# Optimization experiments

Hardware: AMD Instinct MI355X
Metric: run time of the kernel (lower is better)

## Reference

```python
import jax, jax.numpy as jnp
import numpy as np

N = 50000      # nodes
E = 800000     # edges (before self-loops)
F_IN = 256     # input features
HID = 32       # per-head hidden channels, conv1
H1 = 4         # heads conv1 (concat)
H2 = 4         # heads conv2 (mean)
NCLS = 40      # output classes
NEG_SLOPE = 0.2
SM_EPS = 1e-16  # PyG softmax denominator eps
LN_EPS = 1e-5


def setup_inputs() -> dict:
    key = jax.random.key(0)
    ks = jax.random.split(key, 12)
    s1 = 1.0 / np.sqrt(F_IN)
    s2 = 1.0 / np.sqrt(H1 * HID)
    return {
        "x": jax.random.normal(ks[0], (N, F_IN), dtype=jnp.float32),
        "edge_index": jax.random.randint(ks[1], (2, E), 0, N, dtype=jnp.int32),
        "W1": jax.random.normal(ks[2], (F_IN, H1 * HID), dtype=jnp.float32) * s1,
        "att_src1": jax.random.normal(ks[3], (H1, HID), dtype=jnp.float32) * s1,
        "att_dst1": jax.random.normal(ks[4], (H1, HID), dtype=jnp.float32) * s1,
        "b1": jnp.zeros((H1 * HID,), jnp.float32),
        "W2": jax.random.normal(ks[5], (H1 * HID, H2 * NCLS), dtype=jnp.float32) * s2,
        "att_src2": jax.random.normal(ks[6], (H2, NCLS), dtype=jnp.float32) * s2,
        "att_dst2": jax.random.normal(ks[7], (H2, NCLS), dtype=jnp.float32) * s2,
        "b2": jnp.zeros((NCLS,), jnp.float32),
        "ln0_g": jnp.ones((H1 * HID,), jnp.float32),
        "ln0_b": jnp.zeros((H1 * HID,), jnp.float32),
        "ln1_g": jnp.ones((NCLS,), jnp.float32),
        "ln1_b": jnp.zeros((NCLS,), jnp.float32),
    }


def gat_conv(x, edge_index, W, a_src, a_dst, bias, heads, ch, concat):
    """PyG GATConv: self-loops, edge attention, per-dst segment softmax, scatter-sum."""
    n = x.shape[0]
    loops = jnp.arange(n, dtype=edge_index.dtype)
    src = jnp.concatenate([edge_index[0], loops])  # message source
    dst = jnp.concatenate([edge_index[1], loops])  # aggregation target
    h = (x @ W).reshape(n, heads, ch)              # [N,H,C]
    e_src = jnp.einsum('nhc,hc->nh', h, a_src)     # [N,H]
    e_dst = jnp.einsum('nhc,hc->nh', h, a_dst)
    e = jax.nn.leaky_relu(e_src[src] + e_dst[dst], NEG_SLOPE)  # [E',H]
    m = jax.ops.segment_max(e, dst, num_segments=n)            # stable softmax max
    p = jnp.exp(e - m[dst])
    denom = jax.ops.segment_sum(p, dst, num_segments=n)
    alpha = p / (denom[dst] + SM_EPS)                          # [E',H]
    out = jax.ops.segment_sum(h[src] * alpha[:, :, None], dst, num_segments=n)  # [N,H,C]
    out = out.reshape(n, heads * ch) if concat else out.mean(axis=1)
    return out + bias


def layer_norm(x, g, b):
    mu = x.mean(axis=-1, keepdims=True)
    var = jnp.mean((x - mu) ** 2, axis=-1, keepdims=True)
    return (x - mu) * jax.lax.rsqrt(var + LN_EPS) * g + b


def reference(x, edge_index, W1, att_src1, att_dst1, b1, W2, att_src2, att_dst2, b2,
              ln0_g, ln0_b, ln1_g, ln1_b):
    # eval mode: dropout = identity
    h = gat_conv(x, edge_index, W1, att_src1, att_dst1, b1, H1, HID, True)
    h = layer_norm(jax.nn.elu(h), ln0_g, ln0_b)
    h = gat_conv(h, edge_index, W2, att_src2, att_dst2, b2, H2, NCLS, False)
    h = layer_norm(h, ln1_g, ln1_b)
    return jax.nn.log_softmax(h, axis=1)
```

## Files before the change

kernel.cpp:

```cpp
#include <hip/hip_runtime.h>
#include <hip/hip_bf16.h>
#include <hip/hip_fp16.h>

#define NNODES 50000
#define NEDGES 800000
#define FIN    256
#define HEADS  4
#define C1     32
#define D1     128
#define C2     40
#define D2     160
#define CAP    64

#define RB1 144
#define RB2 88
#define ZB  ((NNODES + 255) / 256)
#define FB  (NEDGES / 256)
#define GB1 ((NNODES + 63) / 64)

typedef unsigned short u16;
typedef short v8s __attribute__((ext_vector_type(8)));
typedef float v4f __attribute__((ext_vector_type(4)));

__device__ __forceinline__ float bf2f(unsigned u) {
    union { unsigned u; float f; } x; x.u = u << 16; return x.f;
}
__device__ __forceinline__ u16 f2bf(float f) {
    unsigned u = __float_as_uint(f);
    return (u16)((u + 0x7fff + ((u >> 16) & 1)) >> 16);
}
__device__ __forceinline__ unsigned pk_bf16(float a, float b) {
    unsigned ua = (__float_as_uint(a) + 0x8000u) >> 16;
    unsigned ub = (__float_as_uint(b) + 0x8000u) & 0xffff0000u;
    return ub | ua;
}
__device__ __forceinline__ float wave_sum(float v) {
    #pragma unroll
    for (int m = 32; m > 0; m >>= 1) v += __shfl_xor(v, m, 64);
    return v;
}
__device__ __forceinline__ void wave_sum2(float& a, float& b) {
    #pragma unroll
    for (int m = 32; m > 0; m >>= 1) {
        a += __shfl_xor(a, m, 64);
        b += __shfl_xor(b, m, 64);
    }
}
__device__ __forceinline__ float leaky(float x) { return fmaxf(x, 0.2f * x); }

__device__ __forceinline__ void repack_body(const float* __restrict__ W,
                                            const float* __restrict__ as,
                                            const float* __restrict__ ad,
                                            u16* __restrict__ Wf,
                                            int K, int N, int C, int total, int idx) {
    if (idx >= total) return;
    int KS = K >> 5, NT = N >> 4;
    int j = idx & 7, lane = (idx >> 3) & 63;
    int rest = idx >> 9;
    int ks = rest % KS, nt = rest / KS;
    int k = ks * 32 + (lane >> 4) * 8 + j;
    int n16 = lane & 15;
    float val = 0.f;
    if (nt < NT) {
        val = W[(size_t)k * N + nt * 16 + n16];
    } else if (n16 < 8) {
        int h = n16 & 3;
        const float* av = (n16 < 4) ? as : ad;
        float s = 0.f;
        for (int c = 0; c < C; c++) s += W[(size_t)k * N + h * C + c] * av[h * C + c];
        val = s;
    }
    Wf[idx] = f2bf(val);
}

template <bool AF32, int KK, int NT>
__device__ __forceinline__ void gemm_body(const void* __restrict__ Aptr,
                                          const u16* __restrict__ Wf,
                                          u16* __restrict__ Out,
                                          float* __restrict__ ssrc,
                                          float* __restrict__ sdst, int M, int bid) {
    const int KS = KK / 32;
    const int NCOL = NT * 16;
    int wid = threadIdx.x >> 6, lane = threadIdx.x & 63;
    int r0 = bid * 64 + wid * 16;
    int m = lane & 15, quad = lane >> 4;
    int row = r0 + m;
    bool rowok = row < M;

    v8s a[KS];
    if (AF32) {
        const float* ap = (const float*)Aptr + (size_t)(rowok ? row : 0) * KK + quad * 8;
        #pragma unroll
        for (int ks = 0; ks < KS; ks++) {
            if (rowok) {
                float4 fa = *(const float4*)(ap + ks * 32);
                float4 fb = *(const float4*)(ap + ks * 32 + 4);
                union { unsigned u[4]; v8s v; } c;
                c.u[0] = pk_bf16(fa.x, fa.y); c.u[1] = pk_bf16(fa.z, fa.w);
                c.u[2] = pk_bf16(fb.x, fb.y); c.u[3] = pk_bf16(fb.z, fb.w);
                a[ks] = c.v;
            } else {
                a[ks] = (v8s){0,0,0,0,0,0,0,0};
            }
        }
    } else {
        const u16* ap = (const u16*)Aptr + (size_t)(rowok ? row : 0) * KK + quad * 8;
        #pragma unroll
        for (int ks = 0; ks < KS; ks++)
            a[ks] = rowok ? *(const v8s*)(ap + ks * 32) : (v8s){0,0,0,0,0,0,0,0};
    }

    const v8s* bp0 = (const v8s*)Wf + lane;
    #pragma unroll 2
    for (int nt = 0; nt < NT; nt++) {
        v4f acc = {0.f, 0.f, 0.f, 0.f};
        const v8s* bp = bp0 + nt * KS * 64;
        #pragma unroll
        for (int ks = 0; ks < KS; ks++)
            acc = __builtin_amdgcn_mfma_f32_16x16x32_bf16(a[ks], bp[ks * 64], acc, 0, 0, 0);
        int col = nt * 16 + m;
        #pragma unroll
        for (int reg = 0; reg < 4; reg++) {
            int r = r0 + quad * 4 + reg;
            if (r < M) Out[(size_t)r * NCOL + col] = f2bf(acc[reg]);
        }
    }
    {
        v4f acc = {0.f, 0.f, 0.f, 0.f};
        const v8s* bp = bp0 + NT * KS * 64;
        #pragma unroll
        for (int ks = 0; ks < KS; ks++)
            acc = __builtin_amdgcn_mfma_f32_16x16x32_bf16(a[ks], bp[ks * 64], acc, 0, 0, 0);
        if (m < 8) {
            float* tgt = (m < 4) ? ssrc : sdst;
            int h = m & 3;
            #pragma unroll
            for (int reg = 0; reg < 4; reg++) {
                int r = r0 + quad * 4 + reg;
                if (r < M) tgt[r * 4 + h] = acc[reg];
            }
        }
    }
}

__global__ __launch_bounds__(256) void repack_init(const float* __restrict__ W1,
                                                   const float* __restrict__ as1,
                                                   const float* __restrict__ ad1,
                                                   u16* __restrict__ Wf1,
                                                   const float* __restrict__ W2,
                                                   const float* __restrict__ as2,
                                                   const float* __restrict__ ad2,
                                                   u16* __restrict__ Wf2,
                                                   int* __restrict__ cursor,
                                                   u16* __restrict__ esrc) {
    int b = blockIdx.x;
    if (b < RB1) {
        repack_body(W1, as1, ad1, Wf1, FIN, D1, C1, 9 * 8 * 512, b * 256 + threadIdx.x);
    } else if (b < RB1 + RB2) {
        repack_body(W2, as2, ad2, Wf2, D1, D2, C2, 11 * 4 * 512, (b - RB1) * 256 + threadIdx.x);
    } else {
        int t = (b - RB1 - RB2) * 256 + threadIdx.x;
        if (t < NNODES) { cursor[t] = 1; esrc[t * CAP] = (u16)t; }
    }
}

__global__ __launch_bounds__(256) void gemm1_fill(const float* __restrict__ x,
                                                  const u16* __restrict__ Wf1,
                                                  u16* __restrict__ BH1,
                                                  float* __restrict__ ssrc,
                                                  float* __restrict__ sdst,
                                                  const int* __restrict__ ei,
                                                  int* __restrict__ cursor,
                                                  u16* __restrict__ esrc) {
    if (blockIdx.x < GB1) {
        gemm_body<true, FIN, 8>(x, Wf1, BH1, ssrc, sdst, NNODES, blockIdx.x);
    } else {
        int t = (blockIdx.x - GB1) * 256 + threadIdx.x;
        if (t >= NEDGES) return;
        int s = ei[t], d = ei[NEDGES + t];
        int pos = atomicAdd(&cursor[d], 1);
        esrc[d * CAP + pos] = (u16)s;
    }
}

template <int KK, int NT>
__global__ __launch_bounds__(256) void gemm_mfma(const u16* __restrict__ A,
                                                 const u16* __restrict__ Wf,
                                                 u16* __restrict__ Out,
                                                 float* __restrict__ ssrc,
                                                 float* __restrict__ sdst, int M) {
    gemm_body<false, KK, NT>(A, Wf, Out, ssrc, sdst, M, blockIdx.x);
}

#define PHASE_A32(SRC_ARR, P_ARR)                                                  \
    int nj = end - tb; if (nj > 32) nj = 32;                                       \
    bool on1 = jj < nj, on2 = jj + 16 < nj;                                        \
    int sE1 = on1 ? (int)esrc[tb + jj] : 0;                                        \
    int sE2 = on2 ? (int)esrc[tb + 16 + jj] : 0;                                   \
    if (hh == 0) { if (on1) SRC_ARR[wid][jj] = sE1;                                \
                   if (on2) SRC_ARR[wid][16 + jj] = sE2; }                         \
    float pa = on1 ? __expf(leaky(ssrc[sE1 * 4 + hh] + sdh)) : 0.f;                \
    float pb = on2 ? __expf(leaky(ssrc[sE2 * 4 + hh] + sdh)) : 0.f;                \
    float tsum = pa + pb;                                                          \
    tsum += __shfl_xor(tsum, 1, 64); tsum += __shfl_xor(tsum, 2, 64);              \
    tsum += __shfl_xor(tsum, 4, 64); tsum += __shfl_xor(tsum, 8, 64);              \
    den += tsum;                                                                   \
    if (on1) P_ARR[wid][hh][jj] = pa;                                              \
    if (on2) P_ARR[wid][hh][16 + jj] = pb;

__global__ __launch_bounds__(256) void gat_fused1(const int* __restrict__ cnt,
                                                  const u16* __restrict__ esrc,
                                                  const float* __restrict__ ssrc,
                                                  const float* __restrict__ sdst,
                                                  const u16* __restrict__ BH,
                                                  const float* __restrict__ b1,
                                                  const float* __restrict__ g,
                                                  const float* __restrict__ be,
                                                  u16* __restrict__ BOb) {
    __shared__ int   s_src[4][32];
    __shared__ float s_p[4][4][32];
    __shared__ float s_den[4][4];
    int wid = threadIdx.x >> 6, lane = threadIdx.x & 63;
    int node = blockIdx.x * 4 + wid;
    int jj = lane & 15, hh = lane >> 4;
    int l8 = lane & 15, grp = lane >> 4;
    int head = l8 >> 2;
    float sdh = sdst[node * 4 + hh];
    int beg = node * CAP, end = beg + cnt[node];
    float den = 0.f;
    float acc[8];
    #pragma unroll
    for (int i = 0; i < 8; i++) acc[i] = 0.f;

    for (int tb = beg; tb < end; tb += 32) {
        PHASE_A32(s_src, s_p)
        #pragma unroll 8
        for (int j = grp; j < nj; j += 4) {
            int sj = s_src[wid][j];
            float al = s_p[wid][head][j];
            uint4 h = *(const uint4*)(BH + (size_t)sj * D1 + l8 * 8);
            acc[0] += al * bf2f(h.x & 0xffffu); acc[1] += al * bf2f(h.x >> 16);
            acc[2] += al * bf2f(h.y & 0xffffu); acc[3] += al * bf2f(h.y >> 16);
            acc[4] += al * bf2f(h.z & 0xffffu); acc[5] += al * bf2f(h.z >> 16);
            acc[6] += al * bf2f(h.w & 0xffffu); acc[7] += al * bf2f(h.w >> 16);
        }
    }
    if (jj == 0) s_den[wid][hh] = den;
    #pragma unroll
    for (int i = 0; i < 8; i++) {
        acc[i] += __shfl_xor(acc[i], 16, 64);
        acc[i] += __shfl_xor(acc[i], 32, 64);
    }
    float rden = 1.f / s_den[wid][head];
    float4 bA = *(const float4*)(b1 + l8 * 8), bB = *(const float4*)(b1 + l8 * 8 + 4);
    float v[8];
    v[0] = acc[0] * rden + bA.x; v[1] = acc[1] * rden + bA.y;
    v[2] = acc[2] * rden + bA.z; v[3] = acc[3] * rden + bA.w;
    v[4] = acc[4] * rden + bB.x; v[5] = acc[5] * rden + bB.y;
    v[6] = acc[6] * rden + bB.z; v[7] = acc[7] * rden + bB.w;
    float s8 = 0.f, q8 = 0.f;
    #pragma unroll
    for (int i = 0; i < 8; i++) {
        v[i] = v[i] > 0.f ? v[i] : __expf(v[i]) - 1.f;
        s8 += v[i]; q8 += v[i] * v[i];
    }
    wave_sum2(s8, q8);
    float mu = s8 * (1.f / 512.f);
    float var = q8 * (1.f / 512.f) - mu * mu;
    float rs = rsqrtf(var + 1e-5f);
    if (grp == 0) {
        float4 gA = *(const float4*)(g + l8 * 8),  gB = *(const float4*)(g + l8 * 8 + 4);
        float4 eA = *(const float4*)(be + l8 * 8), eB = *(const float4*)(be + l8 * 8 + 4);
        u16 o[8] = {f2bf((v[0] - mu) * rs * gA.x + eA.x), f2bf((v[1] - mu) * rs * gA.y + eA.y),
                    f2bf((v[2] - mu) * rs * gA.z + eA.z), f2bf((v[3] - mu) * rs * gA.w + eA.w),
                    f2bf((v[4] - mu) * rs * gB.x + eB.x), f2bf((v[5] - mu) * rs * gB.y + eB.y),
                    f2bf((v[6] - mu) * rs * gB.z + eB.z), f2bf((v[7] - mu) * rs * gB.w + eB.w)};
        *(uint4*)(BOb + (size_t)node * D1 + l8 * 8) = *(uint4*)o;
    }
}

__global__ __launch_bounds__(256) void gat_fused2(const int* __restrict__ cnt,
                                                  const u16* __restrict__ esrc,
                                                  const float* __restrict__ ssrc,
                                                  const float* __restrict__ sdst,
                                                  const u16* __restrict__ BH,
                                                  const float* __restrict__ b2,
                                                  const float* __restrict__ g,
                                                  const float* __restrict__ be,
                                                  float* __restrict__ out) {
    __shared__ int   s_src[4][32];
    __shared__ float s_p[4][4][32];
    __shared__ float s_den[4][4];
    __shared__ float scr3[4][3][160];
    int wid = threadIdx.x >> 6, lane = threadIdx.x & 63;
    int node = blockIdx.x * 4 + wid;
    int jj = lane & 15, hh = lane >> 4;
    int grp = lane / 20;
    int glane = lane - grp * 20;
    int head = glane / 5;
    float sdh = sdst[node * 4 + hh];
    int beg = node * CAP, end = beg + cnt[node];
    float den = 0.f;
    float acc[8];
    #pragma unroll
    for (int i = 0; i < 8; i++) acc[i] = 0.f;

    for (int tb = beg; tb < end; tb += 32) {
        PHASE_A32(s_src, s_p)
        if (grp < 3) {
            #pragma unroll 4
            for (int j = grp; j < nj; j += 3) {
                int sj = s_src[wid][j];
                float al = s_p[wid][head][j];
                uint4 h = *(const uint4*)(BH + (size_t)sj * D2 + glane * 8);
                acc[0] += al * bf2f(h.x & 0xffffu); acc[1] += al * bf2f(h.x >> 16);
                acc[2] += al * bf2f(h.y & 0xffffu); acc[3] += al * bf2f(h.y >> 16);
                acc[4] += al * bf2f(h.z & 0xffffu); acc[5] += al * bf2f(h.z >> 16);
                acc[6] += al * bf2f(h.w & 0xffffu); acc[7] += al * bf2f(h.w >> 16);
            }
        }
    }
    if (jj == 0) s_den[wid][hh] = den;
    if (grp < 3) {
        float rden = 1.f / s_den[wid][head];
        float4 oA = {acc[0] * rden, acc[1] * rden, acc[2] * rden, acc[3] * rden};
        float4 oB = {acc[4] * rden, acc[5] * rden, acc[6] * rden, acc[7] * rden};
        *(float4*)&scr3[wid][grp][glane * 8]     = oA;
        *(float4*)&scr3[wid][grp][glane * 8 + 4] = oB;
    }
    bool act = lane < 40;
    int c = act ? lane : 0;
    float o = 0.f;
    if (act) {
        float s = 0.f;
        #pragma unroll
        for (int k = 0; k < 4; k++)
            #pragma unroll
            for (int gg = 0; gg < 3; gg++) s += scr3[wid][gg][c + 40 * k];
        o = 0.25f * s + b2[c];
    }
    float so = act ? o : 0.f, qo = so * o;
    wave_sum2(so, qo);
    float mu = so * (1.f / 40.f);
    float var = qo * (1.f / 40.f) - mu * mu;
    float rs = rsqrtf(var + 1e-5f);
    float y = act ? (o - mu) * rs * g[c] + be[c] : 0.f;
    float ex = act ? __expf(y) : 0.f;
    float lse = __logf(wave_sum(ex));
    if (act) out[(size_t)node * 40 + c] = y - lse;
}

extern "C" void kernel_launch(void* const* d_in, const int* in_sizes, int n_in,
                              void* d_out, int out_size, void* d_ws, size_t ws_size,
                              hipStream_t stream) {
    const float* x   = (const float*)d_in[0];
    const int*   ei  = (const int*)d_in[1];
    const float* W1  = (const float*)d_in[2];
    const float* as1 = (const float*)d_in[3];
    const float* ad1 = (const float*)d_in[4];
    const float* b1  = (const float*)d_in[5];
    const float* W2  = (const float*)d_in[6];
    const float* as2 = (const float*)d_in[7];
    const float* ad2 = (const float*)d_in[8];
    const float* b2  = (const float*)d_in[9];
    const float* g0  = (const float*)d_in[10];
    const float* be0 = (const float*)d_in[11];
    const float* g1  = (const float*)d_in[12];
    const float* be1 = (const float*)d_in[13];

    float* ws = (float*)d_ws;
    u16*   BH1    = (u16*)ws;
    u16*   BH2    = (u16*)ws;
    u16*   BOb    = (u16*)(ws + 4000000);
    float* ssrc   = ws + 7200000;
    float* sdst   = ws + 7400000;
    u16*   esrc   = (u16*)(ws + 7600000);
    int*   cursor = (int*)(ws + 9200000);
    u16*   Wf1    = (u16*)(ws + 9250000);
    u16*   Wf2    = (u16*)(ws + 9268432);

    const int nb4 = NNODES / 4;

    repack_init<<<RB1 + RB2 + ZB, 256, 0, stream>>>(W1, as1, ad1, Wf1,
                                                    W2, as2, ad2, Wf2, cursor, esrc);
    gemm1_fill<<<GB1 + FB, 256, 0, stream>>>(x, Wf1, BH1, ssrc, sdst, ei, cursor, esrc);
    gat_fused1<<<nb4, 256, 0, stream>>>(cursor, esrc, ssrc, sdst, BH1, b1, g0, be0, BOb);
    gemm_mfma<D1, 10><<<GB1, 256, 0, stream>>>(BOb, Wf2, BH2, ssrc, sdst, NNODES);
    gat_fused2<<<nb4, 256, 0, stream>>>(cursor, esrc, ssrc, sdst, BH2, b2, g1, be1, (float*)d_out);
}
```

Before: 264.8 us.

## Fuse second-layer GEMM into first GAT aggregation kernel via per-wave MFMA

Removes the separate gemm_mfma launch for layer 2. Each wave in gat_fused1 now takes its normalized 128-wide bf16 row, spreads it across lanes with shuffles into MFMA A-fragments, and multiplies it by the prepacked W2 to write BH2 and the layer-2 attention scores directly. This drops the BOb round trip through global memory and one kernel launch. In exchange, every wave redoes a small 1-row GEMM with 16-row MFMA tiles, wasting most of each tile and rereading W2 from cache per node. Separate ssrc2/sdst2 buffers are added so layer-1 scores are not overwritten while still in use.

```diff
diff --git a/kernel.cpp b/kernel.cpp
--- a/kernel.cpp
+++ b/kernel.cpp
@@ -183,15 +183,6 @@
     }
 }
 
-template <int KK, int NT>
-__global__ __launch_bounds__(256) void gemm_mfma(const u16* __restrict__ A,
-                                                 const u16* __restrict__ Wf,
-                                                 u16* __restrict__ Out,
-                                                 float* __restrict__ ssrc,
-                                                 float* __restrict__ sdst, int M) {
-    gemm_body<false, KK, NT>(A, Wf, Out, ssrc, sdst, M, blockIdx.x);
-}
-
 #define PHASE_A32(SRC_ARR, P_ARR)                                                  \
     int nj = end - tb; if (nj > 32) nj = 32;                                       \
     bool on1 = jj < nj, on2 = jj + 16 < nj;                                        \
@@ -216,7 +207,10 @@
                                                   const float* __restrict__ b1,
                                                   const float* __restrict__ g,
                                                   const float* __restrict__ be,
-                                                  u16* __restrict__ BOb) {
+                                                  const u16* __restrict__ Wf2,
+                                                  u16* __restrict__ BH2,
+                                                  float* __restrict__ ssrc2,
+                                                  float* __restrict__ sdst2) {
     __shared__ int   s_src[4][32];
     __shared__ float s_p[4][4][32];
     __shared__ float s_den[4][4];
@@ -268,14 +262,46 @@
     float mu = s8 * (1.f / 512.f);
     float var = q8 * (1.f / 512.f) - mu * mu;
     float rs = rsqrtf(var + 1e-5f);
-    if (grp == 0) {
-        float4 gA = *(const float4*)(g + l8 * 8),  gB = *(const float4*)(g + l8 * 8 + 4);
-        float4 eA = *(const float4*)(be + l8 * 8), eB = *(const float4*)(be + l8 * 8 + 4);
-        u16 o[8] = {f2bf((v[0] - mu) * rs * gA.x + eA.x), f2bf((v[1] - mu) * rs * gA.y + eA.y),
-                    f2bf((v[2] - mu) * rs * gA.z + eA.z), f2bf((v[3] - mu) * rs * gA.w + eA.w),
-                    f2bf((v[4] - mu) * rs * gB.x + eB.x), f2bf((v[5] - mu) * rs * gB.y + eB.y),
-                    f2bf((v[6] - mu) * rs * gB.z + eB.z), f2bf((v[7] - mu) * rs * gB.w + eB.w)};
-        *(uint4*)(BOb + (size_t)node * D1 + l8 * 8) = *(uint4*)o;
+
+    float4 gA = *(const float4*)(g + l8 * 8),  gB = *(const float4*)(g + l8 * 8 + 4);
+    float4 eA = *(const float4*)(be + l8 * 8), eB = *(const float4*)(be + l8 * 8 + 4);
+    float y[8];
+    y[0] = (v[0] - mu) * rs * gA.x + eA.x; y[1] = (v[1] - mu) * rs * gA.y + eA.y;
+    y[2] = (v[2] - mu) * rs * gA.z + eA.z; y[3] = (v[3] - mu) * rs * gA.w + eA.w;
+    y[4] = (v[4] - mu) * rs * gB.x + eB.x; y[5] = (v[5] - mu) * rs * gB.y + eB.y;
+    y[6] = (v[6] - mu) * rs * gB.z + eB.z; y[7] = (v[7] - mu) * rs * gB.w + eB.w;
+    unsigned cpack[4];
+    #pragma unroll
+    for (int t = 0; t < 4; t++)
+        cpack[t] = (unsigned)f2bf(y[2 * t]) | ((unsigned)f2bf(y[2 * t + 1]) << 16);
+
+    union { unsigned u[4]; v8s v; } afr[4];
+    #pragma unroll
+    for (int ks = 0; ks < 4; ks++)
+        #pragma unroll
+        for (int t = 0; t < 4; t++)
+            afr[ks].u[t] = __shfl(cpack[t], ks * 4 + grp, 64);
+
+    const v8s* bp0 = (const v8s*)Wf2 + lane;
+    #pragma unroll 2
+    for (int nt = 0; nt < 10; nt++) {
+        v4f a2 = {0.f, 0.f, 0.f, 0.f};
+        const v8s* bp = bp0 + nt * 4 * 64;
+        #pragma unroll
+        for (int ks = 0; ks < 4; ks++)
+            a2 = __builtin_amdgcn_mfma_f32_16x16x32_bf16(afr[ks].v, bp[ks * 64], a2, 0, 0, 0);
+        if (grp == 0) BH2[(size_t)node * D2 + nt * 16 + l8] = f2bf(a2[0]);
+    }
+    {
+        v4f a2 = {0.f, 0.f, 0.f, 0.f};
+        const v8s* bp = bp0 + 10 * 4 * 64;
+        #pragma unroll
+        for (int ks = 0; ks < 4; ks++)
+            a2 = __builtin_amdgcn_mfma_f32_16x16x32_bf16(afr[ks].v, bp[ks * 64], a2, 0, 0, 0);
+        if (grp == 0 && l8 < 8) {
+            float* tgt = (l8 < 4) ? ssrc2 : sdst2;
+            tgt[node * 4 + (l8 & 3)] = a2[0];
+        }
     }
 }
 
@@ -370,21 +396,23 @@
 
     float* ws = (float*)d_ws;
     u16*   BH1    = (u16*)ws;
-    u16*   BH2    = (u16*)ws;
-    u16*   BOb    = (u16*)(ws + 4000000);
+    u16*   BH2    = (u16*)(ws + 3200000);
     float* ssrc   = ws + 7200000;
     float* sdst   = ws + 7400000;
-    u16*   esrc   = (u16*)(ws + 7600000);
-    int*   cursor = (int*)(ws + 9200000);
-    u16*   Wf1    = (u16*)(ws + 9250000);
-    u16*   Wf2    = (u16*)(ws + 9268432);
+    float* ssrc2  = ws + 7600000;
+    float* sdst2  = ws + 7800000;
+    u16*   esrc   = (u16*)(ws + 8000000);
+    int*   cursor = (int*)(ws + 9600000);
+    u16*   Wf1    = (u16*)(ws + 9650000);
+    u16*   Wf2    = (u16*)(ws + 9668432);
 
     const int nb4 = NNODES / 4;
 
     repack_init<<<RB1 + RB2 + ZB, 256, 0, stream>>>(W1, as1, ad1, Wf1,
                                                     W2, as2, ad2, Wf2, cursor, esrc);
     gemm1_fill<<<GB1 + FB, 256, 0, stream>>>(x, Wf1, BH1, ssrc, sdst, ei, cursor, esrc);
-    gat_fused1<<<nb4, 256, 0, stream>>>(cursor, esrc, ssrc, sdst, BH1, b1, g0, be0, BOb);
-    gemm_mfma<D1, 10><<<GB1, 256, 0, stream>>>(BOb, Wf2, BH2, ssrc, sdst, NNODES);
-    gat_fused2<<<nb4, 256, 0, stream>>>(cursor, esrc, ssrc, sdst, BH2, b2, g1, be1, (float*)d_out);
-}
+    gat_fused1<<<nb4, 256, 0, stream>>>(cursor, esrc, ssrc, sdst, BH1, b1, g0, be0,
+                                        Wf2, BH2, ssrc2, sdst2);
+    gat_fused2<<<nb4, 256, 0, stream>>>(cursor, esrc, ssrc2, sdst2, BH2, b2, g1, be1,
+                                        (float*)d_out);
+}
```

Result: slower. 308.2 us (+16.4%).
